# Optimization experiments

Measured on AMD Instinct MI355X. Metric: run time of the kernel, lower is better.

Reference implementation:

```python
import jax, jax.numpy as jnp
import numpy as np

B, C, L = 4, 512, 4096
LN_EPS = 1e-5


def setup_inputs() -> dict:
    key = jax.random.key(0)
    ks = jax.random.split(key, 6)
    s = 1.0 / np.sqrt(C)
    return {
        "x": jax.random.normal(ks[0], (B, C, L), dtype=jnp.float32),
        "ln_w": jnp.ones((C,), dtype=jnp.float32),
        "ln_b": jnp.zeros((C,), dtype=jnp.float32),
        "wq": jax.random.normal(ks[1], (C, C), dtype=jnp.float32) * s,
        "bq": jnp.zeros((C,), dtype=jnp.float32),
        "wk": jax.random.normal(ks[2], (C, C), dtype=jnp.float32) * s,
        "bk": jnp.zeros((C,), dtype=jnp.float32),
        "wv": jax.random.normal(ks[3], (C, C), dtype=jnp.float32) * s,
        "bv": jnp.zeros((C,), dtype=jnp.float32),
        "wp": jax.random.normal(ks[4], (C, C), dtype=jnp.float32) * s,
        "bp": jnp.zeros((C,), dtype=jnp.float32),
    }


def reference(x, ln_w, ln_b, wq, bq, wk, bk, wv, bv, wp, bp):
    # x: [b, c, l]. LayerNorm over channels (permute -> LN -> permute back).
    xt = jnp.swapaxes(x, 1, 2)  # [b, l, c]
    mu = jnp.mean(xt, axis=-1, keepdims=True)
    var = jnp.var(xt, axis=-1, keepdims=True)
    h = (xt - mu) * jax.lax.rsqrt(var + LN_EPS) * ln_w + ln_b  # [b, l, c]

    # 1x1 convs == channel-mixing matmuls (weight [out, in])
    q = jnp.einsum('blc,oc->blo', h, wq) + bq  # [b, l, c]
    k = jnp.einsum('blc,oc->blo', h, wk) + bk
    v = jnp.einsum('blc,oc->blo', h, wv) + bv

    c = x.shape[1]
    scores = jnp.einsum('blc,bmc->blm', q, k) * (float(c) ** -0.5)  # [b, l_q, l_k]
    attn = jax.nn.softmax(scores, axis=-1)
    o = jnp.einsum('blm,bmc->blc', attn, v)  # [b, l, c]

    o = jnp.einsum('blc,oc->blo', o, wp) + bp
    o = jax.nn.selu(o)
    return x + jnp.swapaxes(o, 1, 2)  # [b, c, l]
```

## Files before the change

### kernel.cpp

```cpp
#include <hip/hip_runtime.h>


typedef __attribute__((ext_vector_type(8))) __bf16 bf16x8;
typedef __attribute__((ext_vector_type(4))) __bf16 bf16x4;
typedef __attribute__((ext_vector_type(4))) float  f32x4;

__device__ __forceinline__ f32x4 mfma16(bf16x8 a, bf16x8 b, f32x4 c) {
  return __builtin_amdgcn_mfma_f32_16x16x32_bf16(a, b, c, 0, 0, 0);
}

__device__ __forceinline__ void gll16(const void* g, void* l) {
  __builtin_amdgcn_global_load_lds(
      (const __attribute__((address_space(1))) unsigned int*)g,
      (__attribute__((address_space(3))) unsigned int*)l, 16, 0, 0);
}

__device__ __forceinline__ float selu_f(float v) {
  return 1.0507009873554805f * (v > 0.f ? v : 1.6732632423543772f * (__expf(v) - 1.f));
}

#define QSCALE ((float)(1.4426950408889634 / 22.627416997969522))

__global__ __launch_bounds__(256) void ln_cvt(
    const float* __restrict__ x, const float* __restrict__ lw,
    const float* __restrict__ lb, __bf16* __restrict__ h,
    const float* __restrict__ w0, const float* __restrict__ w1,
    const float* __restrict__ w2, const float* __restrict__ w3,
    __bf16* __restrict__ wdst) {
  __shared__ float xf[512][33];
  __shared__ float red[32][8][4][2];
  __shared__ float smu[32], srs[32];
  const int id = blockIdx.x, tid = threadIdx.x;

  if (id >= 512) {
    int idx = (id - 512) * 256 + tid;
    int which = idx >> 16;
    const float* s = which == 0 ? w0 : which == 1 ? w1 : which == 2 ? w2 : w3;
    f32x4 v = *(const f32x4*)(s + (size_t)(idx & 65535) * 4);
    bf16x4 o = {(__bf16)v.x, (__bf16)v.y, (__bf16)v.z, (__bf16)v.w};
    *(bf16x4*)(wdst + (size_t)idx * 4) = o;
    return;
  }

  const int b = id >> 7, l0 = (id & 127) * 32;
  const int hi = tid >> 3, lq = tid & 7;

  {
    const float* xp = x + (size_t)b * 2097152 + l0 + lq * 4;
    float s[4] = {0.f, 0.f, 0.f, 0.f}, qq[4] = {0.f, 0.f, 0.f, 0.f};
#pragma unroll
    for (int it = 0; it < 16; ++it) {
      int c = it * 32 + hi;
      f32x4 v = *(const f32x4*)(xp + (size_t)c * 4096);
#pragma unroll
      for (int k = 0; k < 4; ++k) {
        s[k] += v[k];
        qq[k] += v[k] * v[k];
        xf[c][lq * 4 + k] = v[k];
      }
    }
#pragma unroll
    for (int k = 0; k < 4; ++k) {
      red[hi][lq][k][0] = s[k];
      red[hi][lq][k][1] = qq[k];
    }
  }
  __syncthreads();
  if (tid < 32) {
    int l4 = tid >> 2, k = tid & 3;
    float S = 0.f, Q = 0.f;
#pragma unroll
    for (int hh = 0; hh < 32; ++hh) {
      S += red[hh][l4][k][0];
      Q += red[hh][l4][k][1];
    }
    float m = S * (1.f / 512.f);
    float var = Q * (1.f / 512.f) - m * m;
    smu[tid] = m;
    srs[tid] = rsqrtf(var + 1e-5f);
  }
  __syncthreads();

#pragma unroll
  for (int l = 0; l < 32; ++l) {
    float m = smu[l], r = srs[l];
#pragma unroll
    for (int st = 0; st < 2; ++st) {
      int c = st * 256 + tid;
      float v = (xf[c][l] - m) * r * lw[c] + lb[c];
      h[((size_t)b * 4096 + l0 + l) * 512 + c] = (__bf16)v;
    }
  }
}

__global__ __launch_bounds__(256, 2) void gemm_qkv(
    const __bf16* __restrict__ A, const __bf16* __restrict__ W,
    const float* __restrict__ b0, const float* __restrict__ b1,
    const float* __restrict__ b2, __bf16* __restrict__ out,
    __bf16* __restrict__ vt) {
  __shared__ __align__(16) __bf16 smem[2 * 128 * 128];
  __bf16* As = smem;
  __bf16* Bs = smem + 16384;
  const int tid = threadIdx.x;
  const int w = tid >> 6, lane = tid & 63, g = lane >> 4, li = lane & 15;
  const int id = blockIdx.x;
  const int jj = id >> 3;
  const int m0 = (16 * (id & 7) + jj / 12) * 128;
  const int n0 = (jj % 12) * 128;
  const int wm = w >> 1, wn = w & 1;
  const int srow = lane >> 4;
  f32x4 acc[4][4] = {};
  for (int kt = 0; kt < 4; ++kt) {
    __syncthreads();
#pragma unroll
    for (int qq = 0; qq < 8; ++qq) {
      int r = w * 32 + qq * 4;
      int gr = (lane & 15) ^ (4 * (qq & 1) + srow);
      gll16(A + (size_t)(m0 + r + srow) * 512 + kt * 128 + gr * 8, &As[r * 128]);
      gll16(W + (size_t)(n0 + r + srow) * 512 + kt * 128 + gr * 8, &Bs[r * 128]);
    }
    __syncthreads();
#pragma unroll
    for (int kk = 0; kk < 4; ++kk) {
      bf16x8 af[4], bf[4];
#pragma unroll
      for (int t = 0; t < 4; ++t) {
        int ra = wm * 64 + t * 16 + li;
        af[t] = *(const bf16x8*)&As[ra * 128 + ((kk * 32 + 8 * g) ^ ((ra & 7) * 8))];
        int rb = wn * 64 + t * 16 + li;
        bf[t] = *(const bf16x8*)&Bs[rb * 128 + ((kk * 32 + 8 * g) ^ ((rb & 7) * 8))];
      }
#pragma unroll
      for (int i = 0; i < 4; ++i)
#pragma unroll
        for (int j = 0; j < 4; ++j) acc[i][j] = mfma16(af[i], bf[j], acc[i][j]);
    }
  }
  const int which = n0 >> 9;
  __syncthreads();
  if (which < 2) {
    const float* bb = which == 0 ? b0 : b1;
    const float sc = which == 0 ? QSCALE : 1.0f;
#pragma unroll
    for (int i = 0; i < 4; ++i) {
#pragma unroll
      for (int j = 0; j < 4; ++j) {
        int rl = wm * 64 + i * 16 + 4 * g;
        int cl = wn * 64 + j * 16 + li;
        float bv = bb[(n0 & 511) + cl];
#pragma unroll
        for (int e = 0; e < 4; ++e)
          smem[(rl + e) * 128 + cl] = (__bf16)((acc[i][j][e] + bv) * sc);
      }
    }
    __syncthreads();
    __bf16* o = out + (size_t)which * 8388608;
#pragma unroll
    for (int rep = 0; rep < 8; ++rep) {
      int ii = rep * 256 + tid;
      int row = ii >> 4, col8 = (ii & 15) * 8;
      *(bf16x8*)&o[(size_t)(m0 + row) * 512 + (n0 & 511) + col8] =
          *(const bf16x8*)&smem[row * 128 + col8];
    }
  } else {
#pragma unroll
    for (int i = 0; i < 4; ++i) {
#pragma unroll
      for (int j = 0; j < 4; ++j) {
        int rl = wm * 64 + i * 16 + 4 * g;
        int cl = wn * 64 + j * 16 + li;
        float bv = b2[(n0 & 511) + cl];
        bf16x4 pk = {(__bf16)(acc[i][j][0] + bv), (__bf16)(acc[i][j][1] + bv),
                     (__bf16)(acc[i][j][2] + bv), (__bf16)(acc[i][j][3] + bv)};
        *(bf16x4*)&smem[cl * 136 + rl] = pk;
      }
    }
    __syncthreads();
    const int bb_ = m0 >> 12, l0_ = m0 & 4095;
#pragma unroll
    for (int rep = 0; rep < 8; ++rep) {
      int chan = rep * 16 + (tid >> 4);
      int l8 = (tid & 15) * 8;
      *(bf16x8*)&vt[((size_t)(bb_ * 512) + (n0 & 511) + chan) * 4096 + l0_ + l8] =
          *(const bf16x8*)&smem[chan * 136 + l8];
    }
  }
}

__global__ __launch_bounds__(256, 2) void gemm_pp(
    const __bf16* __restrict__ A, const __bf16* __restrict__ Bm,
    const float* __restrict__ bias, const float* __restrict__ xres,
    float* __restrict__ out) {
  __shared__ __align__(16) __bf16 As[128 * 128];
  __shared__ __align__(16) __bf16 Bs[128 * 128];
  const int tid = threadIdx.x;
  const int w = tid >> 6, lane = tid & 63, g = lane >> 4, li = lane & 15;
  const int id = blockIdx.x;
  const int jj = id >> 3;
  const int n0 = (16 * (id & 7) + (jj & 15)) * 128;
  const int m0 = (jj >> 4) * 128;
  const int wm = w >> 1, wn = w & 1;
  const int srow = lane >> 4;
  f32x4 acc[4][4] = {};
  for (int kt = 0; kt < 4; ++kt) {
    __syncthreads();
#pragma unroll
    for (int qq = 0; qq < 8; ++qq) {
      int r = w * 32 + qq * 4;
      int gr = (lane & 15) ^ (4 * (qq & 1) + srow);
      gll16(A + (size_t)(m0 + r + srow) * 512 + kt * 128 + gr * 8, &As[r * 128]);
      gll16(Bm + (size_t)(n0 + r + srow) * 512 + kt * 128 + gr * 8, &Bs[r * 128]);
    }
    __syncthreads();
#pragma unroll
    for (int kk = 0; kk < 4; ++kk) {
      bf16x8 af[4], bf[4];
#pragma unroll
      for (int t = 0; t < 4; ++t) {
        int ra = wm * 64 + t * 16 + li;
        af[t] = *(const bf16x8*)&As[ra * 128 + ((kk * 32 + 8 * g) ^ ((ra & 7) * 8))];
        int rb = wn * 64 + t * 16 + li;
        bf[t] = *(const bf16x8*)&Bs[rb * 128 + ((kk * 32 + 8 * g) ^ ((rb & 7) * 8))];
      }
#pragma unroll
      for (int i = 0; i < 4; ++i)
#pragma unroll
        for (int j = 0; j < 4; ++j) acc[i][j] = mfma16(af[i], bf[j], acc[i][j]);
    }
  }
#pragma unroll
  for (int i = 0; i < 4; ++i) {
#pragma unroll
    for (int j = 0; j < 4; ++j) {
      int r = m0 + wm * 64 + i * 16 + 4 * g;
      int c = n0 + wn * 64 + j * 16 + li;
      int bb = c >> 12, l = c & 4095;
#pragma unroll
      for (int e = 0; e < 4; ++e) {
        float v = acc[i][j][e] + bias[r + e];
        size_t oi = ((size_t)bb * 512 + (r + e)) * 4096 + l;
        out[oi] = xres[oi] + selu_f(v);
      }
    }
  }
}

__global__ __launch_bounds__(512, 2) void flash_half(
    const __bf16* __restrict__ Q, const __bf16* __restrict__ K,
    const __bf16* __restrict__ VT, __bf16* __restrict__ Op,
    float* __restrict__ stats) {
  __shared__ __align__(16) __bf16 Ks[64][512];
  __shared__ __align__(16) __bf16 VTs[512][64];
  __shared__ __align__(16) __bf16 Ps[128][64];

  const int tid = threadIdx.x;
  const int w = tid >> 6, lane = tid & 63, g = lane >> 4, li = lane & 15;
  const int id = blockIdx.x;
  const int grp = id & 7;
  const int b = grp >> 1, half = grp & 1;
  const int q0 = (id >> 3) * 128;
  const size_t base = (size_t)b * (4096 * 512);
  const int kvbase = half * 2048;

  bf16x8 qf[16];
  {
    const __bf16* qp = Q + base + (size_t)(q0 + 16 * w + li) * 512 + 8 * g;
#pragma unroll
    for (int ks = 0; ks < 16; ++ks) qf[ks] = *(const bf16x8*)(qp + ks * 32);
  }

  f32x4 acc[8][4] = {};
  f32x4 lacc = {};
  bf16x8 ones;
#pragma unroll
  for (int j = 0; j < 8; ++j) ones[j] = (__bf16)1.0f;

  auto stageK = [&](int kt) {
#pragma unroll
    for (int i = 0; i < 8; ++i) {
      int r = w * 8 + i;
      int y = (lane * 16) ^ ((r & 7) << 4);
      gll16(K + base + (size_t)(kvbase + kt * 64 + r) * 512 + (y >> 1),
            &Ks[r][0]);
    }
  };
  auto stageVT = [&](int kt) {
    const int drow = lane >> 3;
    const int gr = (lane & 7) ^ drow;
#pragma unroll
    for (int i = 0; i < 8; ++i) {
      int d0 = w * 64 + i * 8;
      gll16(VT + (size_t)b * 2097152 + (size_t)(d0 + drow) * 4096 +
                kvbase + kt * 64 + gr * 8,
            &VTs[d0][0]);
    }
  };

  stageK(0);
  stageVT(0);
  __syncthreads();

  for (int kt = 0; kt < 32; ++kt) {
    __builtin_amdgcn_s_setprio(1);
    f32x4 s[4] = {};
#pragma unroll
    for (int ks = 0; ks < 16; ++ks) {
      int e = (ks * 32 + 8 * g) ^ ((li & 7) * 8);
#pragma unroll
      for (int kvt = 0; kvt < 4; ++kvt) {
        bf16x8 kf = *(const bf16x8*)&Ks[kvt * 16 + li][e];
        s[kvt] = mfma16(qf[ks], kf, s[kvt]);
      }
    }
    __builtin_amdgcn_s_setprio(0);

#pragma unroll
    for (int kvt = 0; kvt < 4; ++kvt) {
#pragma unroll
      for (int e = 0; e < 4; ++e) {
        float p = exp2f(s[kvt][e]);
        int row = 16 * w + 4 * g + e;
        int slot = (2 * kvt + (li >> 3)) ^ (row & 7);
        Ps[row][slot * 8 + (li & 7)] = (__bf16)p;
      }
    }
    __syncthreads();

    if (kt + 1 < 32) stageK(kt + 1);

#pragma unroll
    for (int ks = 0; ks < 2; ++ks) {
      bf16x8 bfr[4];
#pragma unroll
      for (int ct = 0; ct < 4; ++ct) {
        int dcol = 64 * w + 16 * ct + li;
        int slot = (4 * ks + g) ^ (li & 7);
        bfr[ct] = *(const bf16x8*)&VTs[dcol][slot * 8];
      }
      __builtin_amdgcn_s_setprio(1);
#pragma unroll
      for (int rt = 0; rt < 8; ++rt) {
        int prow = rt * 16 + li;
        int slot = (4 * ks + g) ^ (li & 7);
        bf16x8 af = *(const bf16x8*)&Ps[prow][slot * 8];
        if (rt == w) lacc = mfma16(af, ones, lacc);
#pragma unroll
        for (int ct = 0; ct < 4; ++ct)
          acc[rt][ct] = mfma16(af, bfr[ct], acc[rt][ct]);
      }
      __builtin_amdgcn_s_setprio(0);
    }
    __syncthreads();

    if (kt + 1 < 32) stageVT(kt + 1);
  }

  if (li == 0)
    *(f32x4*)(stats + half * 16384 + b * 4096 + q0 + 16 * w + 4 * g) = lacc;

  __bf16* C = &Ps[0][0];
  for (int rt = 0; rt < 8; ++rt) {
    __syncthreads();
#pragma unroll
    for (int ct = 0; ct < 4; ++ct)
#pragma unroll
      for (int e = 0; e < 4; ++e)
        C[(4 * g + e) * 512 + 64 * w + 16 * ct + li] = (__bf16)acc[rt][ct][e];
    __syncthreads();
#pragma unroll
    for (int rep = 0; rep < 2; ++rep) {
      int ii = rep * 512 + tid;
      int row16 = ii >> 6, col8 = (ii & 63) * 8;
      *(bf16x8*)&Op[(size_t)half * 8388608 + base +
                    (size_t)(q0 + rt * 16 + row16) * 512 + col8] =
          *(const bf16x8*)&C[row16 * 512 + col8];
    }
  }
}

__global__ __launch_bounds__(256) void combine2(const __bf16* __restrict__ Op,
                                                const float* __restrict__ stats,
                                                __bf16* __restrict__ ao) {
  int gid = blockIdx.x * 256 + threadIdx.x;
  int row = gid >> 6;
  int c = (gid & 63) * 8;
  float l0 = stats[row], l1 = stats[16384 + row];
  float inv = 1.f / (l0 + l1);
  bf16x8 v0 = *(const bf16x8*)(Op + (size_t)row * 512 + c);
  bf16x8 v1 = *(const bf16x8*)(Op + 8388608 + (size_t)row * 512 + c);
  bf16x8 o;
#pragma unroll
  for (int j = 0; j < 8; ++j)
    o[j] = (__bf16)(((float)v0[j] + (float)v1[j]) * inv);
  *(bf16x8*)(ao + (size_t)row * 512 + c) = o;
}

extern "C" void kernel_launch(void* const* d_in, const int* in_sizes, int n_in,
                              void* d_out, int out_size, void* d_ws, size_t ws_size,
                              hipStream_t stream) {
  const float* x   = (const float*)d_in[0];
  const float* lnw = (const float*)d_in[1];
  const float* lnb = (const float*)d_in[2];
  const float* wq  = (const float*)d_in[3];
  const float* bq  = (const float*)d_in[4];
  const float* wk  = (const float*)d_in[5];
  const float* bk  = (const float*)d_in[6];
  const float* wv  = (const float*)d_in[7];
  const float* bv  = (const float*)d_in[8];
  const float* wp  = (const float*)d_in[9];
  const float* bp  = (const float*)d_in[10];

  char* ws = (char*)d_ws;
  const size_t MB = 1024 * 1024;
  __bf16* h    = (__bf16*)(ws);
  __bf16* q    = (__bf16*)(ws + 16 * MB);
  __bf16* vt   = (__bf16*)(ws + 48 * MB);
  __bf16* wbf  = (__bf16*)(ws + 64 * MB);
  __bf16* op   = (__bf16*)(ws + 67 * MB);
  float*  stats= (float*)(ws + 99 * MB);
  __bf16* ao   = h;

  ln_cvt<<<1536, 256, 0, stream>>>(x, lnw, lnb, h, wq, wk, wv, wp, wbf);
  gemm_qkv<<<1536, 256, 0, stream>>>(h, wbf, bq, bk, bv, q, vt);
  flash_half<<<256, 512, 0, stream>>>(q, q + 8388608, vt, op, stats);
  combine2<<<4096, 256, 0, stream>>>(op, stats, ao);
  gemm_pp<<<512, 256, 0, stream>>>(wbf + 3 * 262144, ao, bp, x,
                                   (float*)d_out);
}
```

Measured before the change: 280.8 us.

## Fuse split-KV attention combine into output projection GEMM B-tile loads

Removes the separate combine kernel that merged the two flash-attention halves and normalized by the softmax denominator. gemm_pp now loads both partial outputs, sums them, scales by a per-row inverse sum precomputed in shared memory, and writes the swizzled tile to LDS. This saves an intermediate write and read plus a launch. In exchange, B loads become synchronous register loads instead of direct-to-LDS loads, and each partial tile is reread by several blocks.

After: 282.8 us. Within noise of the previous version (+0.7%).

```diff
diff --git a/kernel.cpp b/kernel.cpp
--- a/kernel.cpp
+++ b/kernel.cpp
@@ -188,11 +188,13 @@
 }
 
 __global__ __launch_bounds__(256, 2) void gemm_pp(
-    const __bf16* __restrict__ A, const __bf16* __restrict__ Bm,
+    const __bf16* __restrict__ A, const __bf16* __restrict__ O0,
+    const __bf16* __restrict__ O1, const float* __restrict__ stats,
     const float* __restrict__ bias, const float* __restrict__ xres,
     float* __restrict__ out) {
   __shared__ __align__(16) __bf16 As[128 * 128];
   __shared__ __align__(16) __bf16 Bs[128 * 128];
+  __shared__ float invl[128];
   const int tid = threadIdx.x;
   const int w = tid >> 6, lane = tid & 63, g = lane >> 4, li = lane & 15;
   const int id = blockIdx.x;
@@ -201,6 +203,10 @@
   const int m0 = (jj >> 4) * 128;
   const int wm = w >> 1, wn = w & 1;
   const int srow = lane >> 4;
+  if (tid < 128) {
+    int p = n0 + tid;
+    invl[tid] = 1.f / (stats[p] + stats[16384 + p]);
+  }
   f32x4 acc[4][4] = {};
   for (int kt = 0; kt < 4; ++kt) {
     __syncthreads();
@@ -209,7 +215,17 @@
       int r = w * 32 + qq * 4;
       int gr = (lane & 15) ^ (4 * (qq & 1) + srow);
       gll16(A + (size_t)(m0 + r + srow) * 512 + kt * 128 + gr * 8, &As[r * 128]);
-      gll16(Bm + (size_t)(n0 + r + srow) * 512 + kt * 128 + gr * 8, &Bs[r * 128]);
+      int R = r + srow;
+      int s = lane & 15;
+      size_t goff = (size_t)(n0 + R) * 512 + kt * 128 + gr * 8;
+      bf16x8 v0 = *(const bf16x8*)(O0 + goff);
+      bf16x8 v1 = *(const bf16x8*)(O1 + goff);
+      float iv = invl[R];
+      bf16x8 ov;
+#pragma unroll
+      for (int j = 0; j < 8; ++j)
+        ov[j] = (__bf16)(((float)v0[j] + (float)v1[j]) * iv);
+      *(bf16x8*)&Bs[R * 128 + s * 8] = ov;
     }
     __syncthreads();
 #pragma unroll
@@ -376,23 +392,6 @@
           *(const bf16x8*)&C[row16 * 512 + col8];
     }
   }
-}
-
-__global__ __launch_bounds__(256) void combine2(const __bf16* __restrict__ Op,
-                                                const float* __restrict__ stats,
-                                                __bf16* __restrict__ ao) {
-  int gid = blockIdx.x * 256 + threadIdx.x;
-  int row = gid >> 6;
-  int c = (gid & 63) * 8;
-  float l0 = stats[row], l1 = stats[16384 + row];
-  float inv = 1.f / (l0 + l1);
-  bf16x8 v0 = *(const bf16x8*)(Op + (size_t)row * 512 + c);
-  bf16x8 v1 = *(const bf16x8*)(Op + 8388608 + (size_t)row * 512 + c);
-  bf16x8 o;
-#pragma unroll
-  for (int j = 0; j < 8; ++j)
-    o[j] = (__bf16)(((float)v0[j] + (float)v1[j]) * inv);
-  *(bf16x8*)(ao + (size_t)row * 512 + c) = o;
 }
 
 extern "C" void kernel_launch(void* const* d_in, const int* in_sizes, int n_in,
@@ -418,12 +417,10 @@
   __bf16* wbf  = (__bf16*)(ws + 64 * MB);
   __bf16* op   = (__bf16*)(ws + 67 * MB);
   float*  stats= (float*)(ws + 99 * MB);
-  __bf16* ao   = h;
 
   ln_cvt<<<1536, 256, 0, stream>>>(x, lnw, lnb, h, wq, wk, wv, wp, wbf);
   gemm_qkv<<<1536, 256, 0, stream>>>(h, wbf, bq, bk, bv, q, vt);
   flash_half<<<256, 512, 0, stream>>>(q, q + 8388608, vt, op, stats);
-  combine2<<<4096, 256, 0, stream>>>(op, stats, ao);
-  gemm_pp<<<512, 256, 0, stream>>>(wbf + 3 * 262144, ao, bp, x,
-                                   (float*)d_out);
-}
+  gemm_pp<<<512, 256, 0, stream>>>(wbf + 3 * 262144, op, op + 8388608, stats,
+                                   bp, x, (float*)d_out);
+}
```
